# Performance work log

Measured on AMD Instinct MI355X. Metric: run time of the kernel, lower is better.

The kernel has to match this reference:

```python
import jax, jax.numpy as jnp
import numpy as np

N_NODES = 50000


def gcn_conv(x, W, b, src, dst, num_nodes):
    # GCNConv (PyG defaults): h = D^{-1/2} (A + I) D^{-1/2} x W + b
    h = x @ W  # [N, out_dim]
    deg = jax.ops.segment_sum(jnp.ones(src.shape[0], h.dtype), dst, num_segments=num_nodes)
    dinv = jnp.where(deg > 0, jax.lax.rsqrt(deg), 0.0)
    norm = dinv[src] * dinv[dst]  # [E]
    out = jax.ops.segment_sum(h[src] * norm[:, None], dst, num_segments=num_nodes)
    return out + b


def setup_inputs() -> dict:
    key = jax.random.key(0)
    k1, k2, k3, k4 = jax.random.split(key, 4)
    x = jax.random.normal(k1, (N_NODES, 512), dtype=jnp.float32)
    ei = jax.random.randint(k2, (2, 800000), 0, N_NODES, dtype=jnp.int64)
    # Glorot-like init for GCN linear weights; PyG bias init zeros
    W1 = jax.random.normal(k3, (512, 128), dtype=jnp.float32) * (1.0 / np.sqrt(512))
    b1 = jnp.zeros((128,), dtype=jnp.float32)
    W2 = jax.random.normal(k4, (128, 64), dtype=jnp.float32) * (1.0 / np.sqrt(128))
    b2 = jnp.zeros((64,), dtype=jnp.float32)
    return {"x": x, "ei": ei, "W1": W1, "b1": b1, "W2": W2, "b2": b2}


def reference(x, ei, W1, b1, W2, b2):
    n = x.shape[0]
    loops = jnp.arange(n, dtype=ei.dtype)
    src = jnp.concatenate([ei[0], loops])  # add self-loops (PyG default)
    dst = jnp.concatenate([ei[1], loops])
    h = jax.nn.relu(gcn_conv(x, W1, b1, src, dst, n))
    return jax.nn.relu(gcn_conv(h, W2, b2, src, dst, n))
```

## Files before the change

### kernel.cpp

```cpp
#include <hip/hip_runtime.h>


#define N_FEAT0 512
#define N_FEAT1 128
#define N_FEAT2 64
#define SLACK 64

typedef _Float16 f16x8 __attribute__((ext_vector_type(8)));
typedef float f32x16 __attribute__((ext_vector_type(16)));


__global__ void k_prep(const float* __restrict__ W1, const float* __restrict__ W2,
                       _Float16* __restrict__ Wt, _Float16* __restrict__ Wt2,
                       int* __restrict__ cnt, int n) {
    int idx = blockIdx.x * 256 + threadIdx.x;
    if (idx < 65536) {
        int k = idx >> 7;
        int c = idx & 127;
        Wt[(size_t)c * 512 + k] = (_Float16)W1[idx];
    } else if (idx < 65536 + 8192) {
        int j = idx - 65536;
        int k = j >> 6;
        int c = j & 63;
        Wt2[(size_t)c * 128 + k] = (_Float16)W2[j];
    }
    if (idx < n) cnt[idx] = 0;
}


__global__ void k_count_scatter(const int* __restrict__ src, const int* __restrict__ dst,
                                int* __restrict__ cnt, int* __restrict__ srcs_pad, int E) {
    const int t = blockIdx.x * blockDim.x + threadIdx.x;
    const int base = t * 4;
    if (base + 3 < E) {
        int4 d = *(const int4*)(dst + base);
        int4 s = *(const int4*)(src + base);
        int p0 = atomicAdd(&cnt[d.x], 1);
        int p1 = atomicAdd(&cnt[d.y], 1);
        int p2 = atomicAdd(&cnt[d.z], 1);
        int p3 = atomicAdd(&cnt[d.w], 1);
        if (p0 < SLACK) srcs_pad[(size_t)d.x * SLACK + p0] = s.x;
        if (p1 < SLACK) srcs_pad[(size_t)d.y * SLACK + p1] = s.y;
        if (p2 < SLACK) srcs_pad[(size_t)d.z * SLACK + p2] = s.z;
        if (p3 < SLACK) srcs_pad[(size_t)d.w * SLACK + p3] = s.w;
    } else {
        for (int i = base; i < E; i++) {
            int d = dst[i];
            int p = atomicAdd(&cnt[d], 1);
            if (p < SLACK) srcs_pad[(size_t)d * SLACK + p] = src[i];
        }
    }
}

__global__ __launch_bounds__(256) void k_gemm1_mfma(const float* __restrict__ X,
                                                    const _Float16* __restrict__ Wt,
                                                    const int* __restrict__ cnt,
                                                    _Float16* __restrict__ H, int n) {
    __shared__ __align__(16) _Float16 ah[4][32][8];
    __shared__ __align__(16) _Float16 wh[4][128][8];
    const int tid = threadIdx.x;
    const int lane = tid & 63;
    const int w = tid >> 6;
    const int row0 = blockIdx.x * 32;

    f32x16 acc0 = {};

    const int arow = tid >> 2;
    const int aoct = tid & 3;
    const bool ax = (tid < 128);
    const int gr = row0 + arow;
    const float* xrow = X + (size_t)gr * N_FEAT0 + aoct * 8;

    const int c0 = tid >> 2,          o0 = tid & 3;
    const int c1 = (tid + 256) >> 2,  o1 = tid & 3;
    const _Float16* wp0 = Wt + (size_t)c0 * 512 + o0 * 8;
    const _Float16* wp1 = Wt + (size_t)c1 * 512 + o1 * 8;

    float4 xa, xb;
    f16x8 w0r, w1r;
    if (ax && gr < n) {
        xa = ((const float4*)xrow)[0];
        xb = ((const float4*)xrow)[1];
    } else {
        xa = xb = make_float4(0.f, 0.f, 0.f, 0.f);
    }
    w0r = *(const f16x8*)wp0;
    w1r = *(const f16x8*)wp1;

    for (int k0 = 0; k0 < N_FEAT0; k0 += 32) {
        if (ax) {
            f16x8 hv;
            hv[0] = (_Float16)xa.x; hv[1] = (_Float16)xa.y;
            hv[2] = (_Float16)xa.z; hv[3] = (_Float16)xa.w;
            hv[4] = (_Float16)xb.x; hv[5] = (_Float16)xb.y;
            hv[6] = (_Float16)xb.z; hv[7] = (_Float16)xb.w;
            *(f16x8*)(&ah[aoct][arow][0]) = hv;
        }
        *(f16x8*)(&wh[o0][c0][0]) = w0r;
        *(f16x8*)(&wh[o1][c1][0]) = w1r;
        __syncthreads();

        const int k1 = k0 + 32;
        if (k1 < N_FEAT0) {
            if (ax && gr < n) {
                xa = ((const float4*)(xrow + k1))[0];
                xb = ((const float4*)(xrow + k1))[1];
            }
            w0r = *(const f16x8*)(wp0 + k1);
            w1r = *(const f16x8*)(wp1 + k1);
        }

#pragma unroll
        for (int kb = 0; kb < 2; kb++) {
            const int oct = kb * 2 + (lane >> 5);
            f16x8 a = *(const f16x8*)(&ah[oct][(lane & 31)][0]);
            f16x8 b = *(const f16x8*)(&wh[oct][w * 32 + (lane & 31)][0]);
            acc0 = __builtin_amdgcn_mfma_f32_32x32x16_f16(a, b, acc0, 0, 0, 0);
        }
        __syncthreads();
    }

    const int col = w * 32 + (lane & 31);
#pragma unroll
    for (int rq = 0; rq < 4; rq++)
#pragma unroll
        for (int rr = 0; rr < 4; rr++) {
            const int reg = rq * 4 + rr;
            const int row = row0 + rr + 8 * rq + 4 * (lane >> 5);
            if (row < n) {
                float di = rsqrtf((float)(cnt[row] + 1));
                H[(size_t)row * N_FEAT1 + col] = (_Float16)(acc0[reg] * di);
            }
        }
}

__global__ __launch_bounds__(256) void k_gemm2_mfma(const _Float16* __restrict__ A,
                                                    const _Float16* __restrict__ Wt2,
                                                    const int* __restrict__ cnt,
                                                    _Float16* __restrict__ H2, int n) {
    __shared__ __align__(16) _Float16 ah[16][128][8];
    __shared__ __align__(16) _Float16 bh[16][64][8];
    const int tid = threadIdx.x;
    const int lane = tid & 63;
    const int w = tid >> 6;
    const int row0 = blockIdx.x * 128;

#pragma unroll
    for (int it = 0; it < 8; it++) {
        int u = tid + it * 256;
        int r = u >> 4;
        int o = u & 15;
        int gr = row0 + r;
        f16x8 v = {};
        if (gr < n) v = *(const f16x8*)(A + (size_t)gr * 128 + o * 8);
        *(f16x8*)(&ah[o][r][0]) = v;
    }
#pragma unroll
    for (int it = 0; it < 4; it++) {
        int u = tid + it * 256;
        int c = u >> 4;
        int o = u & 15;
        *(f16x8*)(&bh[o][c][0]) = *(const f16x8*)(Wt2 + (size_t)c * 128 + o * 8);
    }
    __syncthreads();

    f32x16 acc0 = {}, acc1 = {};
#pragma unroll
    for (int s = 0; s < 8; s++) {
        const int oct = s * 2 + (lane >> 5);
        f16x8 a  = *(const f16x8*)(&ah[oct][w * 32 + (lane & 31)][0]);
        f16x8 b0 = *(const f16x8*)(&bh[oct][(lane & 31)][0]);
        f16x8 b1 = *(const f16x8*)(&bh[oct][32 + (lane & 31)][0]);
        acc0 = __builtin_amdgcn_mfma_f32_32x32x16_f16(a, b0, acc0, 0, 0, 0);
        acc1 = __builtin_amdgcn_mfma_f32_32x32x16_f16(a, b1, acc1, 0, 0, 0);
    }

#pragma unroll
    for (int rq = 0; rq < 4; rq++)
#pragma unroll
        for (int rr = 0; rr < 4; rr++) {
            const int row = row0 + w * 32 + rr + 8 * rq + 4 * (lane >> 5);
            if (row < n) {
                const float di = rsqrtf((float)(cnt[row] + 1));
                const int reg = rq * 4 + rr;
                H2[(size_t)row * N_FEAT2 + (lane & 31)] = (_Float16)(acc0[reg] * di);
                H2[(size_t)row * N_FEAT2 + 32 + (lane & 31)] = (_Float16)(acc1[reg] * di);
            }
        }
}


__global__ __launch_bounds__(256) void k_gather128(const int* __restrict__ srcs_pad,
                                                   const int* __restrict__ cnt,
                                                   const _Float16* __restrict__ H,
                                                   const float* __restrict__ bias,
                                                   _Float16* __restrict__ out, int n) {
    const int node = blockIdx.x * 16 + (threadIdx.x >> 4);
    const int li = threadIdx.x & 15;
    if (node >= n) return;
    const f16x8* __restrict__ H8 = (const f16x8*)H;
    f16x8 sv = H8[(size_t)node * 16 + li];
    float a[8];
#pragma unroll
    for (int q = 0; q < 8; q++) a[q] = (float)sv[q];
    const int c = cnt[node];
    const float di = rsqrtf((float)(c + 1));
    const int e = c < SLACK ? c : SLACK;
    const int* __restrict__ sp = srcs_pad + (size_t)node * SLACK;
    int j = 0;
    for (; j + 3 < e; j += 4) {
        int s0 = sp[j], s1 = sp[j + 1], s2 = sp[j + 2], s3 = sp[j + 3];
        f16x8 v0 = H8[(size_t)s0 * 16 + li];
        f16x8 v1 = H8[(size_t)s1 * 16 + li];
        f16x8 v2 = H8[(size_t)s2 * 16 + li];
        f16x8 v3 = H8[(size_t)s3 * 16 + li];
#pragma unroll
        for (int q = 0; q < 8; q++)
            a[q] += ((float)v0[q] + (float)v1[q]) + ((float)v2[q] + (float)v3[q]);
    }
    for (; j < e; j++) {
        f16x8 v0 = H8[(size_t)sp[j] * 16 + li];
#pragma unroll
        for (int q = 0; q < 8; q++) a[q] += (float)v0[q];
    }
    float4 b0 = *(const float4*)(bias + li * 8);
    float4 b1 = *(const float4*)(bias + li * 8 + 4);
    f16x8 r;
    r[0] = (_Float16)fmaxf(a[0] * di + b0.x, 0.f);
    r[1] = (_Float16)fmaxf(a[1] * di + b0.y, 0.f);
    r[2] = (_Float16)fmaxf(a[2] * di + b0.z, 0.f);
    r[3] = (_Float16)fmaxf(a[3] * di + b0.w, 0.f);
    r[4] = (_Float16)fmaxf(a[4] * di + b1.x, 0.f);
    r[5] = (_Float16)fmaxf(a[5] * di + b1.y, 0.f);
    r[6] = (_Float16)fmaxf(a[6] * di + b1.z, 0.f);
    r[7] = (_Float16)fmaxf(a[7] * di + b1.w, 0.f);
    ((f16x8*)out)[(size_t)node * 16 + li] = r;
}

__global__ __launch_bounds__(256) void k_gather64(const int* __restrict__ srcs_pad,
                                                  const int* __restrict__ cnt,
                                                  const _Float16* __restrict__ H,
                                                  const float* __restrict__ bias,
                                                  float* __restrict__ out, int n) {
    const int node = blockIdx.x * 32 + (threadIdx.x >> 3);
    const int li = threadIdx.x & 7;
    if (node >= n) return;
    const f16x8* __restrict__ H8 = (const f16x8*)H;
    f16x8 sv = H8[(size_t)node * 8 + li];
    float a[8];
#pragma unroll
    for (int q = 0; q < 8; q++) a[q] = (float)sv[q];
    const int c = cnt[node];
    const float di = rsqrtf((float)(c + 1));
    const int e = c < SLACK ? c : SLACK;
    const int* __restrict__ sp = srcs_pad + (size_t)node * SLACK;
    int j = 0;
    for (; j + 3 < e; j += 4) {
        int s0 = sp[j], s1 = sp[j + 1], s2 = sp[j + 2], s3 = sp[j + 3];
        f16x8 v0 = H8[(size_t)s0 * 8 + li];
        f16x8 v1 = H8[(size_t)s1 * 8 + li];
        f16x8 v2 = H8[(size_t)s2 * 8 + li];
        f16x8 v3 = H8[(size_t)s3 * 8 + li];
#pragma unroll
        for (int q = 0; q < 8; q++)
            a[q] += ((float)v0[q] + (float)v1[q]) + ((float)v2[q] + (float)v3[q]);
    }
    for (; j < e; j++) {
        f16x8 v0 = H8[(size_t)sp[j] * 8 + li];
#pragma unroll
        for (int q = 0; q < 8; q++) a[q] += (float)v0[q];
    }
    float4 b0 = *(const float4*)(bias + li * 8);
    float4 b1 = *(const float4*)(bias + li * 8 + 4);
    float4 r0, r1;
    r0.x = fmaxf(a[0] * di + b0.x, 0.f);
    r0.y = fmaxf(a[1] * di + b0.y, 0.f);
    r0.z = fmaxf(a[2] * di + b0.z, 0.f);
    r0.w = fmaxf(a[3] * di + b0.w, 0.f);
    r1.x = fmaxf(a[4] * di + b1.x, 0.f);
    r1.y = fmaxf(a[5] * di + b1.y, 0.f);
    r1.z = fmaxf(a[6] * di + b1.z, 0.f);
    r1.w = fmaxf(a[7] * di + b1.w, 0.f);
    float* op = out + (size_t)node * N_FEAT2 + li * 8;
    *(float4*)op = r0;
    *(float4*)(op + 4) = r1;
}


extern "C" void kernel_launch(void* const* d_in, const int* in_sizes, int n_in,
                              void* d_out, int out_size, void* d_ws, size_t ws_size,
                              hipStream_t stream) {
    const float* x  = (const float*)d_in[0];
    const int*   ei = (const int*)d_in[1];
    const float* W1 = (const float*)d_in[2];
    const float* b1 = (const float*)d_in[3];
    const float* W2 = (const float*)d_in[4];
    const float* b2 = (const float*)d_in[5];
    float* out = (float*)d_out;

    const int n = in_sizes[0] / N_FEAT0;
    const int E = in_sizes[1] / 2;
    const int* src = ei;
    const int* dst = ei + E;

    char* p = (char*)d_ws;
    _Float16* h16      = (_Float16*)p;
    _Float16* agg16    = (_Float16*)(p + 12800000);
    _Float16* h2_16    = (_Float16*)(p + 25600000);
    int*      cnt      = (int*)(p + 32000000);
    int*      srcs_pad = (int*)(p + 32200064);
    _Float16* Wt       = (_Float16*)(p + 45000064);
    _Float16* Wt2      = (_Float16*)(p + 45131136);

    const int B = 256;
    const int nprep = (65536 + 8192 > n ? 65536 + 8192 : n);

    k_prep<<<(nprep + B - 1) / B, B, 0, stream>>>(W1, W2, Wt, Wt2, cnt, n);
    k_count_scatter<<<((E + 3) / 4 + B - 1) / B, B, 0, stream>>>(src, dst, cnt, srcs_pad, E);

    k_gemm1_mfma<<<(n + 31) / 32, B, 0, stream>>>(x, Wt, cnt, h16, n);
    k_gather128<<<(n + 15) / 16, B, 0, stream>>>(srcs_pad, cnt, h16, b1, agg16, n);

    k_gemm2_mfma<<<(n + 127) / 128, B, 0, stream>>>(agg16, Wt2, cnt, h2_16, n);
    k_gather64<<<(n + 31) / 32, B, 0, stream>>>(srcs_pad, cnt, h2_16, b2, out, n);
}
```

Before: 147.1 us.

## Fuse edge scatter with first GEMM and move source normalization into gather

Merges the edge count/scatter kernel and the first MFMA GEMM into one launch, with the first G2 blocks doing the edge scatter and the rest doing the GEMM, so the two independent stages can run concurrently. To remove the GEMM's dependence on degree counts, the source-side D^{-1/2} scaling moves from the GEMM epilogue into the gather. The gather now loads cnt[src] and computes an rsqrt per neighbor. The GEMM loop is also unrolled two k-steps at a time so X can be prefetched 64 columns ahead. The trade-off is extra random cnt loads and rsqrt work in the gather, plus more registers in the GEMM.

New measurement: 155.8 us. 5.9% more time.

```diff
diff --git a/kernel.cpp b/kernel.cpp
--- a/kernel.cpp
+++ b/kernel.cpp
@@ -28,40 +28,46 @@
 }
 
 
-__global__ void k_count_scatter(const int* __restrict__ src, const int* __restrict__ dst,
-                                int* __restrict__ cnt, int* __restrict__ srcs_pad, int E) {
-    const int t = blockIdx.x * blockDim.x + threadIdx.x;
-    const int base = t * 4;
-    if (base + 3 < E) {
-        int4 d = *(const int4*)(dst + base);
-        int4 s = *(const int4*)(src + base);
-        int p0 = atomicAdd(&cnt[d.x], 1);
-        int p1 = atomicAdd(&cnt[d.y], 1);
-        int p2 = atomicAdd(&cnt[d.z], 1);
-        int p3 = atomicAdd(&cnt[d.w], 1);
-        if (p0 < SLACK) srcs_pad[(size_t)d.x * SLACK + p0] = s.x;
-        if (p1 < SLACK) srcs_pad[(size_t)d.y * SLACK + p1] = s.y;
-        if (p2 < SLACK) srcs_pad[(size_t)d.z * SLACK + p2] = s.z;
-        if (p3 < SLACK) srcs_pad[(size_t)d.w * SLACK + p3] = s.w;
-    } else {
-        for (int i = base; i < E; i++) {
-            int d = dst[i];
-            int p = atomicAdd(&cnt[d], 1);
-            if (p < SLACK) srcs_pad[(size_t)d * SLACK + p] = src[i];
-        }
-    }
-}
-
-__global__ __launch_bounds__(256) void k_gemm1_mfma(const float* __restrict__ X,
-                                                    const _Float16* __restrict__ Wt,
-                                                    const int* __restrict__ cnt,
-                                                    _Float16* __restrict__ H, int n) {
+__global__ __launch_bounds__(256) void k_fused(const float* __restrict__ X,
+                                               const _Float16* __restrict__ Wt,
+                                               const int* __restrict__ src,
+                                               const int* __restrict__ dst,
+                                               int* __restrict__ cnt,
+                                               int* __restrict__ srcs_pad,
+                                               _Float16* __restrict__ H,
+                                               int n, int E, int G2) {
     __shared__ __align__(16) _Float16 ah[4][32][8];
     __shared__ __align__(16) _Float16 wh[4][128][8];
     const int tid = threadIdx.x;
+
+    if ((int)blockIdx.x < G2) {
+        const int t = blockIdx.x * 256 + tid;
+        const int base = t * 4;
+        if (base + 3 < E) {
+            int4 d = *(const int4*)(dst + base);
+            int4 s = *(const int4*)(src + base);
+            int p0 = atomicAdd(&cnt[d.x], 1);
+            int p1 = atomicAdd(&cnt[d.y], 1);
+            int p2 = atomicAdd(&cnt[d.z], 1);
+            int p3 = atomicAdd(&cnt[d.w], 1);
+            if (p0 < SLACK) srcs_pad[(size_t)d.x * SLACK + p0] = s.x;
+            if (p1 < SLACK) srcs_pad[(size_t)d.y * SLACK + p1] = s.y;
+            if (p2 < SLACK) srcs_pad[(size_t)d.z * SLACK + p2] = s.z;
+            if (p3 < SLACK) srcs_pad[(size_t)d.w * SLACK + p3] = s.w;
+        } else {
+            for (int i = base; i < E; i++) {
+                int d = dst[i];
+                int p = atomicAdd(&cnt[d], 1);
+                if (p < SLACK) srcs_pad[(size_t)d * SLACK + p] = src[i];
+            }
+        }
+        return;
+    }
+
+    const int bid = blockIdx.x - G2;
     const int lane = tid & 63;
     const int w = tid >> 6;
-    const int row0 = blockIdx.x * 32;
+    const int row0 = bid * 32;
 
     f32x16 acc0 = {};
 
@@ -76,49 +82,59 @@
     const _Float16* wp0 = Wt + (size_t)c0 * 512 + o0 * 8;
     const _Float16* wp1 = Wt + (size_t)c1 * 512 + o1 * 8;
 
-    float4 xa, xb;
-    f16x8 w0r, w1r;
-    if (ax && gr < n) {
-        xa = ((const float4*)xrow)[0];
-        xb = ((const float4*)xrow)[1];
-    } else {
-        xa = xb = make_float4(0.f, 0.f, 0.f, 0.f);
-    }
-    w0r = *(const f16x8*)wp0;
-    w1r = *(const f16x8*)wp1;
-
-    for (int k0 = 0; k0 < N_FEAT0; k0 += 32) {
-        if (ax) {
-            f16x8 hv;
-            hv[0] = (_Float16)xa.x; hv[1] = (_Float16)xa.y;
-            hv[2] = (_Float16)xa.z; hv[3] = (_Float16)xa.w;
-            hv[4] = (_Float16)xb.x; hv[5] = (_Float16)xb.y;
-            hv[6] = (_Float16)xb.z; hv[7] = (_Float16)xb.w;
-            *(f16x8*)(&ah[aoct][arow][0]) = hv;
+    float4 xa0, xb0, xa1, xb1;
+    {
+        const float4 z = make_float4(0.f, 0.f, 0.f, 0.f);
+        if (ax && gr < n) {
+            xa0 = ((const float4*)xrow)[0];
+            xb0 = ((const float4*)xrow)[1];
+            xa1 = ((const float4*)(xrow + 32))[0];
+            xb1 = ((const float4*)(xrow + 32))[1];
+        } else {
+            xa0 = z; xb0 = z; xa1 = z; xb1 = z;
         }
-        *(f16x8*)(&wh[o0][c0][0]) = w0r;
-        *(f16x8*)(&wh[o1][c1][0]) = w1r;
-        __syncthreads();
-
-        const int k1 = k0 + 32;
-        if (k1 < N_FEAT0) {
-            if (ax && gr < n) {
-                xa = ((const float4*)(xrow + k1))[0];
-                xb = ((const float4*)(xrow + k1))[1];
-            }
-            w0r = *(const f16x8*)(wp0 + k1);
-            w1r = *(const f16x8*)(wp1 + k1);
-        }
-
-#pragma unroll
-        for (int kb = 0; kb < 2; kb++) {
-            const int oct = kb * 2 + (lane >> 5);
-            f16x8 a = *(const f16x8*)(&ah[oct][(lane & 31)][0]);
-            f16x8 b = *(const f16x8*)(&wh[oct][w * 32 + (lane & 31)][0]);
-            acc0 = __builtin_amdgcn_mfma_f32_32x32x16_f16(a, b, acc0, 0, 0, 0);
-        }
-        __syncthreads();
-    }
+    }
+    f16x8 w0r = *(const f16x8*)wp0;
+    f16x8 w1r = *(const f16x8*)wp1;
+
+#define GCN_STEP(PA, PB, K0)                                                 \
+    {                                                                        \
+        if (ax) {                                                            \
+            f16x8 hv;                                                        \
+            hv[0] = (_Float16)PA.x; hv[1] = (_Float16)PA.y;                  \
+            hv[2] = (_Float16)PA.z; hv[3] = (_Float16)PA.w;                  \
+            hv[4] = (_Float16)PB.x; hv[5] = (_Float16)PB.y;                  \
+            hv[6] = (_Float16)PB.z; hv[7] = (_Float16)PB.w;                  \
+            *(f16x8*)(&ah[aoct][arow][0]) = hv;                              \
+        }                                                                    \
+        *(f16x8*)(&wh[o0][c0][0]) = w0r;                                     \
+        *(f16x8*)(&wh[o1][c1][0]) = w1r;                                     \
+        const int kx = (K0) + 64;                                            \
+        if (kx < N_FEAT0 && ax && gr < n) {                                  \
+            PA = ((const float4*)(xrow + kx))[0];                            \
+            PB = ((const float4*)(xrow + kx))[1];                            \
+        }                                                                    \
+        const int kw = (K0) + 32;                                            \
+        if (kw < N_FEAT0) {                                                  \
+            w0r = *(const f16x8*)(wp0 + kw);                                 \
+            w1r = *(const f16x8*)(wp1 + kw);                                 \
+        }                                                                    \
+        __syncthreads();                                                     \
+        _Pragma("unroll")                                                    \
+        for (int kb = 0; kb < 2; kb++) {                                     \
+            const int oct = kb * 2 + (lane >> 5);                            \
+            f16x8 a = *(const f16x8*)(&ah[oct][(lane & 31)][0]);             \
+            f16x8 b = *(const f16x8*)(&wh[oct][w * 32 + (lane & 31)][0]);    \
+            acc0 = __builtin_amdgcn_mfma_f32_32x32x16_f16(a, b, acc0, 0, 0, 0); \
+        }                                                                    \
+        __syncthreads();                                                     \
+    }
+
+    for (int t2 = 0; t2 < 8; t2++) {
+        GCN_STEP(xa0, xb0, t2 * 64)
+        GCN_STEP(xa1, xb1, t2 * 64 + 32)
+    }
+#undef GCN_STEP
 
     const int col = w * 32 + (lane & 31);
 #pragma unroll
@@ -127,10 +143,8 @@
         for (int rr = 0; rr < 4; rr++) {
             const int reg = rq * 4 + rr;
             const int row = row0 + rr + 8 * rq + 4 * (lane >> 5);
-            if (row < n) {
-                float di = rsqrtf((float)(cnt[row] + 1));
-                H[(size_t)row * N_FEAT1 + col] = (_Float16)(acc0[reg] * di);
-            }
+            if (row < n)
+                H[(size_t)row * N_FEAT1 + col] = (_Float16)acc0[reg];
         }
 }
 
@@ -189,7 +203,6 @@
         }
 }
 
-
 __global__ __launch_bounds__(256) void k_gather128(const int* __restrict__ srcs_pad,
                                                    const int* __restrict__ cnt,
                                                    const _Float16* __restrict__ H,
@@ -200,28 +213,35 @@
     if (node >= n) return;
     const f16x8* __restrict__ H8 = (const f16x8*)H;
     f16x8 sv = H8[(size_t)node * 16 + li];
-    float a[8];
-#pragma unroll
-    for (int q = 0; q < 8; q++) a[q] = (float)sv[q];
     const int c = cnt[node];
     const float di = rsqrtf((float)(c + 1));
+    float a[8];
+#pragma unroll
+    for (int q = 0; q < 8; q++) a[q] = di * (float)sv[q];
     const int e = c < SLACK ? c : SLACK;
     const int* __restrict__ sp = srcs_pad + (size_t)node * SLACK;
     int j = 0;
     for (; j + 3 < e; j += 4) {
         int s0 = sp[j], s1 = sp[j + 1], s2 = sp[j + 2], s3 = sp[j + 3];
+        float d0 = rsqrtf((float)(cnt[s0] + 1));
+        float d1 = rsqrtf((float)(cnt[s1] + 1));
+        float d2 = rsqrtf((float)(cnt[s2] + 1));
+        float d3 = rsqrtf((float)(cnt[s3] + 1));
         f16x8 v0 = H8[(size_t)s0 * 16 + li];
         f16x8 v1 = H8[(size_t)s1 * 16 + li];
         f16x8 v2 = H8[(size_t)s2 * 16 + li];
         f16x8 v3 = H8[(size_t)s3 * 16 + li];
 #pragma unroll
         for (int q = 0; q < 8; q++)
-            a[q] += ((float)v0[q] + (float)v1[q]) + ((float)v2[q] + (float)v3[q]);
+            a[q] += (d0 * (float)v0[q] + d1 * (float)v1[q]) +
+                    (d2 * (float)v2[q] + d3 * (float)v3[q]);
     }
     for (; j < e; j++) {
-        f16x8 v0 = H8[(size_t)sp[j] * 16 + li];
-#pragma unroll
-        for (int q = 0; q < 8; q++) a[q] += (float)v0[q];
+        int s0 = sp[j];
+        float d0 = rsqrtf((float)(cnt[s0] + 1));
+        f16x8 v0 = H8[(size_t)s0 * 16 + li];
+#pragma unroll
+        for (int q = 0; q < 8; q++) a[q] += d0 * (float)v0[q];
     }
     float4 b0 = *(const float4*)(bias + li * 8);
     float4 b1 = *(const float4*)(bias + li * 8 + 4);
@@ -314,13 +334,12 @@
 
     const int B = 256;
     const int nprep = (65536 + 8192 > n ? 65536 + 8192 : n);
+    const int G2 = ((E + 3) / 4 + B - 1) / B;
+    const int G1 = (n + 31) / 32;
 
     k_prep<<<(nprep + B - 1) / B, B, 0, stream>>>(W1, W2, Wt, Wt2, cnt, n);
-    k_count_scatter<<<((E + 3) / 4 + B - 1) / B, B, 0, stream>>>(src, dst, cnt, srcs_pad, E);
-
-    k_gemm1_mfma<<<(n + 31) / 32, B, 0, stream>>>(x, Wt, cnt, h16, n);
+    k_fused<<<G2 + G1, B, 0, stream>>>(x, Wt, src, dst, cnt, srcs_pad, h16, n, E, G2);
     k_gather128<<<(n + 15) / 16, B, 0, stream>>>(srcs_pad, cnt, h16, b1, agg16, n);
-
     k_gemm2_mfma<<<(n + 127) / 128, B, 0, stream>>>(agg16, Wt2, cnt, h2_16, n);
     k_gather64<<<(n + 31) / 32, B, 0, stream>>>(srcs_pad, cnt, h2_16, b2, out, n);
 }
```
